# Kernel tuning notes

Measured on AMD Instinct MI355X. Metric: run time of the kernel, lower is better.

The kernel has to match this reference:

```python
import jax, jax.numpy as jnp
import numpy as np
import math

V, D, H, L, T_MAX = 512, 256, 4, 8, 256
HD = D // H
EPS = 1e-5


def _ln(x, g, b):
    mu = jnp.mean(x, axis=-1, keepdims=True)
    var = jnp.mean(jnp.square(x - mu), axis=-1, keepdims=True)
    return (x - mu) * jax.lax.rsqrt(var + EPS) * g + b


def _pos_encoding(T, D):
    pos = jnp.arange(T, dtype=jnp.float32)[:, None]
    div = jnp.exp(jnp.arange(0, D, 2, dtype=jnp.float32) * (-math.log(10000.0) / D))
    pe = jnp.zeros((T, D), dtype=jnp.float32)
    pe = pe.at[:, 0::2].set(jnp.sin(pos * div))
    pe = pe.at[:, 1::2].set(jnp.cos(pos * div))
    return pe


def setup_inputs() -> dict:
    key = jax.random.key(0)
    ks = jax.random.split(key, 16)
    s = 0.02
    B, T = 128, 256
    return {
        "idx": jax.random.randint(ks[0], (B, T), 0, V),
        "tok_emb": jax.random.normal(ks[1], (V, D)) * s,
        "Wq": jax.random.normal(ks[2], (L, D, D)) * s,
        "Wk": jax.random.normal(ks[3], (L, D, D)) * s,
        "Wv": jax.random.normal(ks[4], (L, D, D)) * s,
        "Wo": jax.random.normal(ks[5], (L, D, D)) * s,
        "bo": jnp.zeros((L, D)),
        "W1": jax.random.normal(ks[6], (L, D, D)) * s,
        "b1": jnp.zeros((L, D)),
        "W2": jax.random.normal(ks[7], (L, D, D)) * s,
        "b2": jnp.zeros((L, D)),
        "g1": jnp.ones((L, D)), "be1": jnp.zeros((L, D)),
        "g2": jnp.ones((L, D)), "be2": jnp.zeros((L, D)),
        "gf": jnp.ones((D,)), "bf": jnp.zeros((D,)),
        "Wh": jax.random.normal(ks[8], (D, V)) * s,
        "bh": jnp.zeros((V,)),
    }


def reference(idx, tok_emb, Wq, Wk, Wv, Wo, bo, W1, b1, W2, b2,
              g1, be1, g2, be2, gf, bf, Wh, bh):
    B, T = idx.shape
    x = tok_emb[idx] + _pos_encoding(T, D)[None]  # [B,T,D]
    causal = jnp.tril(jnp.ones((T, T), dtype=bool))
    scale = D ** (-0.5)  # NOTE: original scales by n_embd, not head_size
    for l in range(L):
        h = _ln(x, g1[l], be1[l])
        q = (h @ Wq[l]).reshape(B, T, H, HD)
        k = (h @ Wk[l]).reshape(B, T, H, HD)
        v = (h @ Wv[l]).reshape(B, T, H, HD)
        wei = jnp.einsum('bqhd,bkhd->bhqk', q, k) * scale
        wei = jnp.where(causal, wei, -jnp.inf)
        wei = jax.nn.softmax(wei, axis=-1)
        att = jnp.einsum('bhqk,bkhd->bqhd', wei, v).reshape(B, T, D)
        x = x + att @ Wo[l] + bo[l]
        h = _ln(x, g2[l], be2[l])
        x = x + jax.nn.relu(h @ W1[l] + b1[l]) @ W2[l] + b2[l]
    x = _ln(x, gf, bf)
    logits = x @ Wh + bh  # [B,T,V]
    return logits
```

## Files before the change

kernel.cpp:

```cpp
#include <hip/hip_runtime.h>
#include <hip/hip_bf16.h>

typedef unsigned short u16;
typedef __attribute__((ext_vector_type(8))) short short8;
typedef __attribute__((ext_vector_type(4))) float f32x4;

#define DEV static __device__ __forceinline__

DEV u16 f2bf(float x){
  union { __hip_bfloat16 b; u16 u; } c;
  c.b = __float2bfloat16(x);
  return c.u;
}

DEV void gload16(const void* g, void* lds){
  __builtin_amdgcn_global_load_lds((const __attribute__((address_space(1))) void*)g,
                                   (__attribute__((address_space(3))) void*)lds, 16, 0, 0);
}

__global__ __launch_bounds__(512)
void wconv_kernel(const float* __restrict__ Wq, const float* __restrict__ Wk,
                  const float* __restrict__ Wv, const float* __restrict__ Wo,
                  const float* __restrict__ W1, const float* __restrict__ W2,
                  const float* __restrict__ Wh,
                  u16* __restrict__ WqkvT, u16* __restrict__ WoT,
                  u16* __restrict__ W1T, u16* __restrict__ W2T, u16* __restrict__ WhT)
{
  __shared__ float tile[64][65];
  const int j = blockIdx.y;
  int N = 256;
  const float* src; u16* dst;
  if (j < 48){
    const int li = j / 6, t = j % 6;
    switch(t){
      case 0:  src = Wq + li*65536; dst = WqkvT + li*196608;          break;
      case 1:  src = Wk + li*65536; dst = WqkvT + li*196608 + 65536;  break;
      case 2:  src = Wv + li*65536; dst = WqkvT + li*196608 + 131072; break;
      case 3:  src = Wo + li*65536; dst = WoT  + li*65536;            break;
      case 4:  src = W1 + li*65536; dst = W1T  + li*65536;            break;
      default: src = W2 + li*65536; dst = W2T  + li*65536;            break;
    }
  } else { N = 512; src = Wh; dst = WhT; }
  const int tilesPerRow = N >> 6;
  if ((int)blockIdx.x >= tilesPerRow * 4) return;
  const int tx = blockIdx.x % tilesPerRow, ty = blockIdx.x / tilesPerRow;
  const int tid = threadIdx.x;
  #pragma unroll
  for (int i=0;i<2;++i){
    const int e = tid + i*512;
    const int r = e >> 4, cq = (e & 15)*4;
    float4 v = *(const float4*)(src + (size_t)(ty*64 + r)*N + tx*64 + cq);
    tile[r][cq+0]=v.x; tile[r][cq+1]=v.y; tile[r][cq+2]=v.z; tile[r][cq+3]=v.w;
  }
  __syncthreads();
  #pragma unroll
  for (int i=0;i<2;++i){
    const int e = tid + i*512;
    const int orow = e >> 4, tq = (e & 15)*4;
    ushort4 o;
    o.x = f2bf(tile[tq+0][orow]); o.y = f2bf(tile[tq+1][orow]);
    o.z = f2bf(tile[tq+2][orow]); o.w = f2bf(tile[tq+3][orow]);
    *(ushort4*)(dst + (size_t)(tx*64 + orow)*256 + ty*64 + tq) = o;
  }
}

__global__ __launch_bounds__(256)
void embed_ln_kernel(const int* __restrict__ idx, const float* __restrict__ emb,
                     const float* __restrict__ g, const float* __restrict__ be,
                     float* __restrict__ x, u16* __restrict__ hb)
{
  const int tid = threadIdx.x;
  const int w = tid >> 6, l = tid & 63;
  const int row = blockIdx.x*4 + w;
  const int t = row & 255;
  const int v = idx[row];
  const int c4 = l*4;
  float4 e = *(const float4*)(emb + (size_t)v*256 + c4);
  float r[4];
  const float ef[4] = {e.x, e.y, e.z, e.w};
  #pragma unroll
  for (int i=0;i<4;++i){
    const int c = c4 + i;
    const float div = expf((float)(c & ~1) * (-9.210340371976184f/256.f));
    const float ang = (float)t * div;
    r[i] = ((c & 1) ? cosf(ang) : sinf(ang)) + ef[i];
  }
  *(float4*)(x + (size_t)row*256 + c4) = (float4){r[0],r[1],r[2],r[3]};
  float s = r[0]+r[1]+r[2]+r[3];
  float q = r[0]*r[0]+r[1]*r[1]+r[2]*r[2]+r[3]*r[3];
  #pragma unroll
  for (int m=32; m; m>>=1){ s += __shfl_xor(s,m); q += __shfl_xor(q,m); }
  const float mu = s * (1.f/256.f);
  const float var = q * (1.f/256.f) - mu*mu;
  const float rstd = rsqrtf(var + 1e-5f);
  const float4 gv = *(const float4*)(g + c4);
  const float4 bv = *(const float4*)(be + c4);
  ushort4 o;
  o.x = f2bf((r[0]-mu)*rstd*gv.x + bv.x);
  o.y = f2bf((r[1]-mu)*rstd*gv.y + bv.y);
  o.z = f2bf((r[2]-mu)*rstd*gv.z + bv.z);
  o.w = f2bf((r[3]-mu)*rstd*gv.w + bv.w);
  *(ushort4*)(hb + (size_t)row*256 + c4) = o;
}

template<bool OBF, bool RELU_, bool BIAS_>
__global__ __launch_bounds__(256)
void gemm_kernel(const u16* __restrict__ A, const u16* __restrict__ W,
                 const float* __restrict__ bias, void* __restrict__ Cv, int ldC)
{
  __shared__ __align__(16) u16 Al[2][4096];
  __shared__ __align__(16) u16 Bl[2][4096];
  const int tid = threadIdx.x;
  const int w = tid >> 6, l = tid & 63;
  const int lr = l & 15, lg = l >> 4;
  const int m0 = blockIdx.x * 128, n0 = blockIdx.y * 128;
  const int wm = w >> 1, wn = w & 1;
  const int rowc = l >> 2;
  const int pswz = (l & 3) ^ ((l >> 3) & 3);

  f32x4 acc[4][4];
  #pragma unroll
  for (int i=0;i<4;++i)
    #pragma unroll
    for (int jn=0;jn<4;++jn) acc[i][jn] = (f32x4){0.f,0.f,0.f,0.f};

  #pragma unroll
  for (int cc=0; cc<2; ++cc){
    const int c = w + cc*4;
    gload16(A + (size_t)(m0 + 16*c + rowc)*256 + pswz*8, &Al[0][c*512]);
    gload16(W + (size_t)(n0 + 16*c + rowc)*256 + pswz*8, &Bl[0][c*512]);
  }
  __syncthreads();

  for (int kt=0; kt<8; ++kt){
    if (kt < 7){
      const int kofs = (kt+1) * 32, nb = (kt+1) & 1;
      #pragma unroll
      for (int cc=0; cc<2; ++cc){
        const int c = w + cc*4;
        gload16(A + (size_t)(m0 + 16*c + rowc)*256 + kofs + pswz*8, &Al[nb][c*512]);
        gload16(W + (size_t)(n0 + 16*c + rowc)*256 + kofs + pswz*8, &Bl[nb][c*512]);
      }
    }
    const int buf = kt & 1;
    short8 af[4], bf[4];
    #pragma unroll
    for (int mt=0; mt<4; ++mt){
      const int row = wm*64 + mt*16 + lr;
      const int kb = (lg*16) ^ ((((row>>1)&3))<<4);
      af[mt] = *(const short8*)((const char*)Al[buf] + row*64 + kb);
    }
    #pragma unroll
    for (int nt=0; nt<4; ++nt){
      const int row = wn*64 + nt*16 + lr;
      const int kb = (lg*16) ^ ((((row>>1)&3))<<4);
      bf[nt] = *(const short8*)((const char*)Bl[buf] + row*64 + kb);
    }
    #pragma unroll
    for (int mt=0; mt<4; ++mt)
      #pragma unroll
      for (int nt=0; nt<4; ++nt)
        acc[mt][nt] = __builtin_amdgcn_mfma_f32_16x16x32_bf16(af[mt], bf[nt], acc[mt][nt], 0,0,0);
    __syncthreads();
  }

  #pragma unroll
  for (int nt=0; nt<4; ++nt){
    const int col = n0 + wn*64 + nt*16 + lr;
    const float bv = BIAS_ ? bias[col] : 0.f;
    #pragma unroll
    for (int mt=0; mt<4; ++mt){
      f32x4 v = acc[mt][nt];
      #pragma unroll
      for (int r=0;r<4;++r){
        const int row = m0 + wm*64 + mt*16 + lg*4 + r;
        float val = v[r] + bv;
        if (RELU_) val = fmaxf(val, 0.f);
        if (OBF) ((u16*)Cv)[(size_t)row*ldC + col] = f2bf(val);
        else     ((float*)Cv)[(size_t)row*ldC + col] = val;
      }
    }
  }
}

__global__ __launch_bounds__(256, 2)
void gemm_res_ln_kernel(const u16* __restrict__ A, const u16* __restrict__ W,
                        const float* __restrict__ bias,
                        const float* __restrict__ g, const float* __restrict__ be,
                        float* __restrict__ x, u16* __restrict__ hb)
{
  __shared__ __align__(16) u16 Al[2][2048];
  __shared__ __align__(16) u16 Bl[2][8192];
  __shared__ float sS[64][2], sQ[64][2];
  const int tid = threadIdx.x;
  const int w = tid >> 6, l = tid & 63;
  const int lr = l & 15, lg = l >> 4;
  const int m0 = blockIdx.x * 64;
  const int wm = w >> 1, wn = w & 1;
  const int rowc = l >> 2;
  const int pswz = (l & 3) ^ ((l >> 3) & 3);

  f32x4 acc[2][2][4];
  #pragma unroll
  for (int p=0;p<2;++p)
    #pragma unroll
    for (int i=0;i<2;++i)
      #pragma unroll
      for (int jn=0;jn<4;++jn) acc[p][i][jn] = (f32x4){0.f,0.f,0.f,0.f};

  gload16(A + (size_t)(m0 + 16*w + rowc)*256 + pswz*8, &Al[0][w*512]);
  #pragma unroll
  for (int cc=0; cc<4; ++cc){
    const int c = w + cc*4;
    gload16(W + (size_t)(16*c + rowc)*256 + pswz*8, &Bl[0][c*512]);
  }
  __syncthreads();

  for (int kt=0; kt<8; ++kt){
    if (kt < 7){
      const int kofs = (kt+1)*32, nb = (kt+1)&1;
      gload16(A + (size_t)(m0 + 16*w + rowc)*256 + kofs + pswz*8, &Al[nb][w*512]);
      #pragma unroll
      for (int cc=0; cc<4; ++cc){
        const int c = w + cc*4;
        gload16(W + (size_t)(16*c + rowc)*256 + kofs + pswz*8, &Bl[nb][c*512]);
      }
    }
    const int buf = kt & 1;
    short8 af[2], bf[2][4];
    #pragma unroll
    for (int mt=0; mt<2; ++mt){
      const int row = wm*32 + mt*16 + lr;
      const int kb = (lg*16) ^ ((((row>>1)&3))<<4);
      af[mt] = *(const short8*)((const char*)Al[buf] + row*64 + kb);
    }
    #pragma unroll
    for (int p=0; p<2; ++p)
      #pragma unroll
      for (int nt=0; nt<4; ++nt){
        const int brow = p*128 + wn*64 + nt*16 + lr;
        const int kb = (lg*16) ^ ((((brow>>1)&3))<<4);
        bf[p][nt] = *(const short8*)((const char*)Bl[buf] + brow*64 + kb);
      }
    #pragma unroll
    for (int p=0; p<2; ++p)
      #pragma unroll
      for (int mt=0; mt<2; ++mt)
        #pragma unroll
        for (int nt=0; nt<4; ++nt)
          acc[p][mt][nt] = __builtin_amdgcn_mfma_f32_16x16x32_bf16(af[mt], bf[p][nt], acc[p][mt][nt], 0,0,0);
    __syncthreads();
  }

  float bcol[2][4], gcol[2][4], becol[2][4];
  #pragma unroll
  for (int p=0;p<2;++p)
    #pragma unroll
    for (int nt=0;nt<4;++nt){
      const int col = p*128 + wn*64 + nt*16 + lr;
      bcol[p][nt] = bias[col]; gcol[p][nt] = g[col]; becol[p][nt] = be[col];
    }
  float s8[2][4], q8[2][4];
  #pragma unroll
  for (int mt=0;mt<2;++mt)
    #pragma unroll
    for (int rr=0;rr<4;++rr){ s8[mt][rr]=0.f; q8[mt][rr]=0.f; }

  #pragma unroll
  for (int p=0;p<2;++p)
    #pragma unroll
    for (int mt=0;mt<2;++mt)
      #pragma unroll
      for (int nt=0;nt<4;++nt)
        #pragma unroll
        for (int rr=0;rr<4;++rr){
          const int row = m0 + wm*32 + mt*16 + lg*4 + rr;
          const int col = p*128 + wn*64 + nt*16 + lr;
          float val = acc[p][mt][nt][rr] + bcol[p][nt] + x[(size_t)row*256 + col];
          x[(size_t)row*256 + col] = val;
          acc[p][mt][nt][rr] = val;
          s8[mt][rr] += val; q8[mt][rr] += val*val;
        }
  #pragma unroll
  for (int mt=0;mt<2;++mt)
    #pragma unroll
    for (int rr=0;rr<4;++rr){
      #pragma unroll
      for (int m=1; m<16; m<<=1){
        s8[mt][rr] += __shfl_xor(s8[mt][rr], m);
        q8[mt][rr] += __shfl_xor(q8[mt][rr], m);
      }
      if (lr == 0){
        const int lrow = wm*32 + mt*16 + lg*4 + rr;
        sS[lrow][wn] = s8[mt][rr]; sQ[lrow][wn] = q8[mt][rr];
      }
    }
  __syncthreads();

  #pragma unroll
  for (int mt=0;mt<2;++mt)
    #pragma unroll
    for (int rr=0;rr<4;++rr){
      const int lrow = wm*32 + mt*16 + lg*4 + rr;
      const float mu = (sS[lrow][0] + sS[lrow][1]) * (1.f/256.f);
      const float var = (sQ[lrow][0] + sQ[lrow][1]) * (1.f/256.f) - mu*mu;
      const float rstd = rsqrtf(var + 1e-5f);
      #pragma unroll
      for (int p=0;p<2;++p)
        #pragma unroll
        for (int nt=0;nt<4;++nt){
          const int col = p*128 + wn*64 + nt*16 + lr;
          const float out = (acc[p][mt][nt][rr] - mu)*rstd*gcol[p][nt] + becol[p][nt];
          hb[(size_t)(m0+lrow)*256 + col] = f2bf(out);
        }
    }
}

__global__ __launch_bounds__(512, 4)
void attn_kernel(const u16* __restrict__ qkv, u16* __restrict__ att)
{
  __shared__ __align__(16) u16 sK[16384];
  __shared__ __align__(16) u16 sV[16384];
  __shared__ __align__(16) u16 sP[8192];
  const int bh = blockIdx.x;
  const int b = bh >> 2, h = bh & 3;
  const int tid = threadIdx.x;
  const int w = tid >> 6, l = tid & 63, lr = l & 15, lg = l >> 4;
  const u16* base = qkv + (size_t)(b*256)*768;

  #pragma unroll
  for (int it=0; it<4; ++it){
    const int c = tid + it*512;
    const int t = c >> 3, p = c & 7;
    uint4 val = *(const uint4*)(base + (size_t)t*768 + 256 + h*64 + p*8);
    *(uint4*)((char*)sK + t*128 + ((p*16) ^ ((t&7)<<4))) = val;
  }
  #pragma unroll
  for (int h2=0; h2<2; ++h2){
    #pragma unroll
    for (int i=0;i<2;++i){
      const int e = tid + i*512;
      const int t2 = e >> 3, p = e & 7;
      uint4 val = *(const uint4*)(base + (size_t)(h2*128 + t2)*768 + 512 + h*64 + p*8);
      *(uint4*)((char*)sP + t2*128 + ((p*16) ^ ((t2&7)<<4))) = val;
    }
    __syncthreads();
    {
      const int tq2 = tid >> 4, hq = tid & 15;
      ushort4 vv[4];
      #pragma unroll
      for (int i=0;i<4;++i){
        const int t2 = tq2*4 + i;
        vv[i] = *(const ushort4*)((char*)sP + t2*128 +
                   (((hq>>1)*16) ^ ((t2&7)<<4)) + (hq&1)*8);
      }
      const int tqg = h2*32 + tq2;
      #pragma unroll
      for (int i2=0;i2<4;++i2){
        const int hd = hq*4 + i2;
        ushort4 o;
        o.x = ((const u16*)&vv[0])[i2]; o.y = ((const u16*)&vv[1])[i2];
        o.z = ((const u16*)&vv[2])[i2]; o.w = ((const u16*)&vv[3])[i2];
        *(ushort4*)((char*)sV + hd*512 + ((tqg*8) ^ ((hd&31)<<4))) = o;
      }
    }
    __syncthreads();
  }

  char* sPw = (char*)sP + w*2048;
  const int swzq = (lr & 7) << 4;
  u16* ab = att + (size_t)(b*256)*256 + h*64;
  const float c1 = 0.09016844005556021f;

  #pragma unroll
  for (int ph=0; ph<2; ++ph){
    const int rt = ph ? (15 - w) : w;
    const u16* qp = base + (size_t)(rt*16 + lr)*768 + h*64;
    const short8 qf0 = *(const short8*)(qp + lg*8);
    const short8 qf1 = *(const short8*)(qp + 32 + lg*8);

    f32x4 acc[16];
    #pragma unroll
    for (int nt=0; nt<16; ++nt) acc[nt] = (f32x4){0.f,0.f,0.f,0.f};
    #pragma unroll
    for (int nt=0; nt<16; ++nt){
      if (nt <= rt){
        const int row = nt*16 + lr;
        const int swz = (row & 7) << 4;
        short8 k0 = *(const short8*)((const char*)sK + row*128 + ((lg*16) ^ swz));
        short8 k1 = *(const short8*)((const char*)sK + row*128 + ((64 + lg*16) ^ swz));
        acc[nt] = __builtin_amdgcn_mfma_f32_16x16x32_bf16(k0, qf0, acc[nt], 0,0,0);
        acc[nt] = __builtin_amdgcn_mfma_f32_16x16x32_bf16(k1, qf1, acc[nt], 0,0,0);
      }
    }
    #pragma unroll
    for (int nt=0; nt<16; ++nt){
      if (nt == rt){
        #pragma unroll
        for (int r=0;r<4;++r)
          acc[nt][r] = (lg*4 + r > lr) ? -3.0e38f : acc[nt][r];
      }
    }

    float m_ = -3.0e38f;
    #pragma unroll
    for (int nt=0; nt<16; ++nt){
      if (nt <= rt){
        float t01 = fmaxf(acc[nt][0], acc[nt][1]);
        float t23 = fmaxf(acc[nt][2], acc[nt][3]);
        m_ = fmaxf(m_, fmaxf(t01, t23));
      }
    }
    m_ = fmaxf(m_, __shfl_xor(m_, 16));
    m_ = fmaxf(m_, __shfl_xor(m_, 32));
    const float mm = m_ * c1;
    float s_ = 0.f;
    #pragma unroll
    for (int nt=0; nt<16; ++nt){
      if (nt <= rt){
        #pragma unroll
        for (int r=0;r<4;++r){
          const float p = exp2f(fmaf(acc[nt][r], c1, -mm));
          acc[nt][r] = p;
          s_ += p;
        }
      }
    }
    s_ += __shfl_xor(s_, 16);
    s_ += __shfl_xor(s_, 32);
    const float inv = 1.f / s_;

    f32x4 oacc[4];
    #pragma unroll
    for (int nt=0; nt<4; ++nt) oacc[nt] = (f32x4){0.f,0.f,0.f,0.f};
    #pragma unroll
    for (int c=0; c<4; ++c){
      if (c <= (rt >> 2)){
        #pragma unroll
        for (int e=0; e<4; ++e){
          const int nt = 4*c + e;
          ushort4 pk;
          #pragma unroll
          for (int r=0;r<4;++r){
            const float val = (nt <= rt) ? acc[nt][r] * inv : 0.f;
            ((u16*)&pk)[r] = f2bf(val);
          }
          *(ushort4*)(sPw + lr*128 + ((e*32 + lg*8) ^ swzq)) = pk;
        }
        #pragma unroll
        for (int kc=0; kc<2; ++kc){
          const int tc = 2*c + kc;
          if (tc <= (rt >> 1)){
            const short8 ap = *(const short8*)(sPw + lr*128 + ((kc*64 + lg*16) ^ swzq));
            #pragma unroll
            for (int nt=0; nt<4; ++nt){
              const int vrow = nt*16 + lr;
              const short8 bv = *(const short8*)((const char*)sV + vrow*512 +
                                   ((tc*64 + lg*16) ^ ((vrow&31)<<4)));
              oacc[nt] = __builtin_amdgcn_mfma_f32_16x16x32_bf16(ap, bv, oacc[nt], 0,0,0);
            }
          }
        }
      }
    }

    #pragma unroll
    for (int nt=0; nt<4; ++nt)
      #pragma unroll
      for (int r=0;r<4;++r){
        const int row = rt*16 + lg*4 + r;
        ab[(size_t)row*256 + nt*16 + lr] = f2bf(oacc[nt][r]);
      }
  }
}

extern "C" void kernel_launch(void* const* d_in, const int* in_sizes, int n_in,
                              void* d_out, int out_size, void* d_ws, size_t ws_size,
                              hipStream_t stream)
{
  (void)in_sizes; (void)n_in; (void)out_size; (void)ws_size;
  const int*   idx = (const int*)  d_in[0];
  const float* tok = (const float*)d_in[1];
  const float* Wq  = (const float*)d_in[2];
  const float* Wk  = (const float*)d_in[3];
  const float* Wv  = (const float*)d_in[4];
  const float* Wo  = (const float*)d_in[5];
  const float* bo  = (const float*)d_in[6];
  const float* W1  = (const float*)d_in[7];
  const float* b1  = (const float*)d_in[8];
  const float* W2  = (const float*)d_in[9];
  const float* b2  = (const float*)d_in[10];
  const float* g1  = (const float*)d_in[11];
  const float* be1 = (const float*)d_in[12];
  const float* g2  = (const float*)d_in[13];
  const float* be2 = (const float*)d_in[14];
  const float* gf  = (const float*)d_in[15];
  const float* bfi = (const float*)d_in[16];
  const float* Wh  = (const float*)d_in[17];
  const float* bh  = (const float*)d_in[18];

  char* ws = (char*)d_ws;
  float* x    = (float*)ws;  ws += (size_t)32768*256*4;
  u16*   hb   = (u16*)ws;    ws += (size_t)32768*256*2;
  u16*   mid  = (u16*)ws;    ws += (size_t)32768*256*2;
  u16*   qkv  = (u16*)ws;    ws += (size_t)32768*768*2;
  u16*   att  = (u16*)ws;    ws += (size_t)32768*256*2;
  u16*   WqkvT= (u16*)ws;    ws += (size_t)8*768*256*2;
  u16*   WoT  = (u16*)ws;    ws += (size_t)8*256*256*2;
  u16*   W1T  = (u16*)ws;    ws += (size_t)8*256*256*2;
  u16*   W2T  = (u16*)ws;    ws += (size_t)8*256*256*2;
  u16*   WhT  = (u16*)ws;    ws += (size_t)512*256*2;

  wconv_kernel<<<dim3(32,49),512,0,stream>>>(Wq,Wk,Wv,Wo,W1,W2,Wh,WqkvT,WoT,W1T,W2T,WhT);
  embed_ln_kernel<<<8192,256,0,stream>>>(idx, tok, g1, be1, x, hb);
  for (int l=0; l<8; ++l){
    gemm_kernel<true,false,false><<<dim3(256,6),256,0,stream>>>(
        hb, WqkvT + (size_t)l*196608, nullptr, qkv, 768);
    attn_kernel<<<512,512,0,stream>>>(qkv, att);
    gemm_res_ln_kernel<<<512,256,0,stream>>>(
        att, WoT + (size_t)l*65536, bo + l*256, g2 + l*256, be2 + l*256, x, hb);
    gemm_kernel<true,true,true><<<dim3(256,2),256,0,stream>>>(
        hb, W1T + (size_t)l*65536, b1 + l*256, mid, 256);
    const float* gn = (l < 7) ? (g1 + (l+1)*256) : gf;
    const float* bn = (l < 7) ? (be1 + (l+1)*256) : bfi;
    gemm_res_ln_kernel<<<512,256,0,stream>>>(
        mid, W2T + (size_t)l*65536, b2 + l*256, gn, bn, x, hb);
  }
  gemm_kernel<false,false,true><<<dim3(256,4),256,0,stream>>>(
      hb, WhT, bh, (float*)d_out, 512);
}
```

Before: 869.0 us.

## Fuse QKV projection into attention kernel, drop qkv buffer round trip

```diff
diff --git a/kernel.cpp b/kernel.cpp
--- a/kernel.cpp
+++ b/kernel.cpp
@@ -317,7 +317,8 @@
 }
 
 __global__ __launch_bounds__(512, 4)
-void attn_kernel(const u16* __restrict__ qkv, u16* __restrict__ att)
+void fused_qkv_attn_kernel(const u16* __restrict__ hb, const u16* __restrict__ Wqkv,
+                           u16* __restrict__ att)
 {
   __shared__ __align__(16) u16 sK[16384];
   __shared__ __align__(16) u16 sV[16384];
@@ -326,46 +327,72 @@
   const int b = bh >> 2, h = bh & 3;
   const int tid = threadIdx.x;
   const int w = tid >> 6, l = tid & 63, lr = l & 15, lg = l >> 4;
-  const u16* base = qkv + (size_t)(b*256)*768;
-
-  #pragma unroll
-  for (int it=0; it<4; ++it){
-    const int c = tid + it*512;
-    const int t = c >> 3, p = c & 7;
-    uint4 val = *(const uint4*)(base + (size_t)t*768 + 256 + h*64 + p*8);
-    *(uint4*)((char*)sK + t*128 + ((p*16) ^ ((t&7)<<4))) = val;
-  }
-  #pragma unroll
-  for (int h2=0; h2<2; ++h2){
-    #pragma unroll
-    for (int i=0;i<2;++i){
-      const int e = tid + i*512;
-      const int t2 = e >> 3, p = e & 7;
-      uint4 val = *(const uint4*)(base + (size_t)(h2*128 + t2)*768 + 512 + h*64 + p*8);
-      *(uint4*)((char*)sP + t2*128 + ((p*16) ^ ((t2&7)<<4))) = val;
-    }
-    __syncthreads();
-    {
-      const int tq2 = tid >> 4, hq = tid & 15;
-      ushort4 vv[4];
-      #pragma unroll
-      for (int i=0;i<4;++i){
-        const int t2 = tq2*4 + i;
-        vv[i] = *(const ushort4*)((char*)sP + t2*128 +
-                   (((hq>>1)*16) ^ ((t2&7)<<4)) + (hq&1)*8);
-      }
-      const int tqg = h2*32 + tq2;
-      #pragma unroll
-      for (int i2=0;i2<4;++i2){
-        const int hd = hq*4 + i2;
-        ushort4 o;
-        o.x = ((const u16*)&vv[0])[i2]; o.y = ((const u16*)&vv[1])[i2];
-        o.z = ((const u16*)&vv[2])[i2]; o.w = ((const u16*)&vv[3])[i2];
-        *(ushort4*)((char*)sV + hd*512 + ((tqg*8) ^ ((hd&31)<<4))) = o;
-      }
-    }
-    __syncthreads();
-  }
+  const u16* hbb = hb + (size_t)(b*256)*256;
+  const u16* Wq_ = Wqkv + (size_t)(h*64)*256;
+  const u16* Wk_ = Wqkv + 65536 + (size_t)(h*64)*256;
+  const u16* Wv_ = Wqkv + 131072 + (size_t)(h*64)*256;
+
+  {
+    f32x4 pacc[4][4];
+    #pragma unroll
+    for (int i=0;i<4;++i)
+      #pragma unroll
+      for (int jn=0;jn<4;++jn) pacc[i][jn] = (f32x4){0.f,0.f,0.f,0.f};
+    if (w < 4){
+      const int t0 = w*64;
+      for (int kt=0; kt<8; ++kt){
+        short8 af[4], bf[4];
+        #pragma unroll
+        for (int mt=0; mt<4; ++mt)
+          af[mt] = *(const short8*)(Wk_ + (size_t)(mt*16+lr)*256 + kt*32 + lg*8);
+        #pragma unroll
+        for (int nt=0; nt<4; ++nt)
+          bf[nt] = *(const short8*)(hbb + (size_t)(t0+nt*16+lr)*256 + kt*32 + lg*8);
+        #pragma unroll
+        for (int mt=0; mt<4; ++mt)
+          #pragma unroll
+          for (int nt=0; nt<4; ++nt)
+            pacc[mt][nt] = __builtin_amdgcn_mfma_f32_16x16x32_bf16(af[mt], bf[nt], pacc[mt][nt], 0,0,0);
+      }
+      #pragma unroll
+      for (int mt=0; mt<4; ++mt)
+        #pragma unroll
+        for (int nt=0; nt<4; ++nt){
+          const int t = t0 + nt*16 + lr;
+          ushort4 o;
+          o.x = f2bf(pacc[mt][nt][0]); o.y = f2bf(pacc[mt][nt][1]);
+          o.z = f2bf(pacc[mt][nt][2]); o.w = f2bf(pacc[mt][nt][3]);
+          *(ushort4*)((char*)sK + t*128 + ((mt*32 + lg*8) ^ ((t&7)<<4))) = o;
+        }
+    } else {
+      const int t0 = (w-4)*64;
+      for (int kt=0; kt<8; ++kt){
+        short8 af[4], bf[4];
+        #pragma unroll
+        for (int mt=0; mt<4; ++mt)
+          af[mt] = *(const short8*)(hbb + (size_t)(t0+mt*16+lr)*256 + kt*32 + lg*8);
+        #pragma unroll
+        for (int nt=0; nt<4; ++nt)
+          bf[nt] = *(const short8*)(Wv_ + (size_t)(nt*16+lr)*256 + kt*32 + lg*8);
+        #pragma unroll
+        for (int mt=0; mt<4; ++mt)
+          #pragma unroll
+          for (int nt=0; nt<4; ++nt)
+            pacc[mt][nt] = __builtin_amdgcn_mfma_f32_16x16x32_bf16(af[mt], bf[nt], pacc[mt][nt], 0,0,0);
+      }
+      #pragma unroll
+      for (int mt=0; mt<4; ++mt)
+        #pragma unroll
+        for (int nt=0; nt<4; ++nt){
+          const int d = nt*16 + lr;
+          ushort4 o;
+          o.x = f2bf(pacc[mt][nt][0]); o.y = f2bf(pacc[mt][nt][1]);
+          o.z = f2bf(pacc[mt][nt][2]); o.w = f2bf(pacc[mt][nt][3]);
+          *(ushort4*)((char*)sV + d*512 + (((t0 + mt*16 + lg*4)*2) ^ ((d&31)<<4))) = o;
+        }
+    }
+  }
+  __syncthreads();
 
   char* sPw = (char*)sP + w*2048;
   const int swzq = (lr & 7) << 4;
@@ -375,9 +402,29 @@
   #pragma unroll
   for (int ph=0; ph<2; ++ph){
     const int rt = ph ? (15 - w) : w;
-    const u16* qp = base + (size_t)(rt*16 + lr)*768 + h*64;
-    const short8 qf0 = *(const short8*)(qp + lg*8);
-    const short8 qf1 = *(const short8*)(qp + 32 + lg*8);
+
+    {
+      f32x4 qacc[4];
+      #pragma unroll
+      for (int mt=0; mt<4; ++mt) qacc[mt] = (f32x4){0.f,0.f,0.f,0.f};
+      for (int kt=0; kt<8; ++kt){
+        const short8 bq = *(const short8*)(hbb + (size_t)(rt*16+lr)*256 + kt*32 + lg*8);
+        #pragma unroll
+        for (int mt=0; mt<4; ++mt){
+          const short8 aq = *(const short8*)(Wq_ + (size_t)(mt*16+lr)*256 + kt*32 + lg*8);
+          qacc[mt] = __builtin_amdgcn_mfma_f32_16x16x32_bf16(aq, bq, qacc[mt], 0,0,0);
+        }
+      }
+      #pragma unroll
+      for (int mt=0; mt<4; ++mt){
+        ushort4 o;
+        o.x = f2bf(qacc[mt][0]); o.y = f2bf(qacc[mt][1]);
+        o.z = f2bf(qacc[mt][2]); o.w = f2bf(qacc[mt][3]);
+        *(ushort4*)(sPw + lr*128 + ((mt*32 + lg*8) ^ swzq)) = o;
+      }
+    }
+    const short8 qf0 = *(const short8*)(sPw + lr*128 + ((lg*16) ^ swzq));
+    const short8 qf1 = *(const short8*)(sPw + lr*128 + ((64 + lg*16) ^ swzq));
 
     f32x4 acc[16];
     #pragma unroll
@@ -503,7 +550,6 @@
   float* x    = (float*)ws;  ws += (size_t)32768*256*4;
   u16*   hb   = (u16*)ws;    ws += (size_t)32768*256*2;
   u16*   mid  = (u16*)ws;    ws += (size_t)32768*256*2;
-  u16*   qkv  = (u16*)ws;    ws += (size_t)32768*768*2;
   u16*   att  = (u16*)ws;    ws += (size_t)32768*256*2;
   u16*   WqkvT= (u16*)ws;    ws += (size_t)8*768*256*2;
   u16*   WoT  = (u16*)ws;    ws += (size_t)8*256*256*2;
@@ -514,9 +560,7 @@
   wconv_kernel<<<dim3(32,49),512,0,stream>>>(Wq,Wk,Wv,Wo,W1,W2,Wh,WqkvT,WoT,W1T,W2T,WhT);
   embed_ln_kernel<<<8192,256,0,stream>>>(idx, tok, g1, be1, x, hb);
   for (int l=0; l<8; ++l){
-    gemm_kernel<true,false,false><<<dim3(256,6),256,0,stream>>>(
-        hb, WqkvT + (size_t)l*196608, nullptr, qkv, 768);
-    attn_kernel<<<512,512,0,stream>>>(qkv, att);
+    fused_qkv_attn_kernel<<<512,512,0,stream>>>(hb, WqkvT + (size_t)l*196608, att);
     gemm_res_ln_kernel<<<512,256,0,stream>>>(
         att, WoT + (size_t)l*65536, bo + l*256, g2 + l*256, be2 + l*256, x, hb);
     gemm_kernel<true,true,true><<<dim3(256,2),256,0,stream>>>(
```

New measurement: 1.076 ms. +23.8%, slower.

## Store residual stream in bf16 and simplify V transpose staging in attention

Applied to the files above, without the earlier changes.

```diff
diff --git a/kernel.cpp b/kernel.cpp
--- a/kernel.cpp
+++ b/kernel.cpp
@@ -11,6 +11,11 @@
   union { __hip_bfloat16 b; u16 u; } c;
   c.b = __float2bfloat16(x);
   return c.u;
+}
+DEV float bf2f(u16 u){
+  union { float f; unsigned i; } c;
+  c.i = ((unsigned)u) << 16;
+  return c.f;
 }
 
 DEV void gload16(const void* g, void* lds){
@@ -67,7 +72,7 @@
 __global__ __launch_bounds__(256)
 void embed_ln_kernel(const int* __restrict__ idx, const float* __restrict__ emb,
                      const float* __restrict__ g, const float* __restrict__ be,
-                     float* __restrict__ x, u16* __restrict__ hb)
+                     u16* __restrict__ x, u16* __restrict__ hb)
 {
   const int tid = threadIdx.x;
   const int w = tid >> 6, l = tid & 63;
@@ -85,7 +90,9 @@
     const float ang = (float)t * div;
     r[i] = ((c & 1) ? cosf(ang) : sinf(ang)) + ef[i];
   }
-  *(float4*)(x + (size_t)row*256 + c4) = (float4){r[0],r[1],r[2],r[3]};
+  ushort4 xo;
+  xo.x = f2bf(r[0]); xo.y = f2bf(r[1]); xo.z = f2bf(r[2]); xo.w = f2bf(r[3]);
+  *(ushort4*)(x + (size_t)row*256 + c4) = xo;
   float s = r[0]+r[1]+r[2]+r[3];
   float q = r[0]*r[0]+r[1]*r[1]+r[2]*r[2]+r[3]*r[3];
   #pragma unroll
@@ -187,7 +194,7 @@
 void gemm_res_ln_kernel(const u16* __restrict__ A, const u16* __restrict__ W,
                         const float* __restrict__ bias,
                         const float* __restrict__ g, const float* __restrict__ be,
-                        float* __restrict__ x, u16* __restrict__ hb)
+                        u16* __restrict__ x, u16* __restrict__ hb)
 {
   __shared__ __align__(16) u16 Al[2][2048];
   __shared__ __align__(16) u16 Bl[2][8192];
@@ -276,8 +283,9 @@
         for (int rr=0;rr<4;++rr){
           const int row = m0 + wm*32 + mt*16 + lg*4 + rr;
           const int col = p*128 + wn*64 + nt*16 + lr;
-          float val = acc[p][mt][nt][rr] + bcol[p][nt] + x[(size_t)row*256 + col];
-          x[(size_t)row*256 + col] = val;
+          float val = acc[p][mt][nt][rr] + bcol[p][nt] + bf2f(x[(size_t)row*256 + col]);
+          x[(size_t)row*256 + col] = f2bf(val);
+          val = bf2f(f2bf(val));
           acc[p][mt][nt][rr] = val;
           s8[mt][rr] += val; q8[mt][rr] += val*val;
         }
@@ -336,36 +344,17 @@
     *(uint4*)((char*)sK + t*128 + ((p*16) ^ ((t&7)<<4))) = val;
   }
   #pragma unroll
-  for (int h2=0; h2<2; ++h2){
-    #pragma unroll
-    for (int i=0;i<2;++i){
-      const int e = tid + i*512;
-      const int t2 = e >> 3, p = e & 7;
-      uint4 val = *(const uint4*)(base + (size_t)(h2*128 + t2)*768 + 512 + h*64 + p*8);
-      *(uint4*)((char*)sP + t2*128 + ((p*16) ^ ((t2&7)<<4))) = val;
-    }
-    __syncthreads();
-    {
-      const int tq2 = tid >> 4, hq = tid & 15;
-      ushort4 vv[4];
-      #pragma unroll
-      for (int i=0;i<4;++i){
-        const int t2 = tq2*4 + i;
-        vv[i] = *(const ushort4*)((char*)sP + t2*128 +
-                   (((hq>>1)*16) ^ ((t2&7)<<4)) + (hq&1)*8);
-      }
-      const int tqg = h2*32 + tq2;
-      #pragma unroll
-      for (int i2=0;i2<4;++i2){
-        const int hd = hq*4 + i2;
-        ushort4 o;
-        o.x = ((const u16*)&vv[0])[i2]; o.y = ((const u16*)&vv[1])[i2];
-        o.z = ((const u16*)&vv[2])[i2]; o.w = ((const u16*)&vv[3])[i2];
-        *(ushort4*)((char*)sV + hd*512 + ((tqg*8) ^ ((hd&31)<<4))) = o;
-      }
-    }
-    __syncthreads();
-  }
+  for (int it=0; it<8; ++it){
+    const int c = tid + it*512;
+    const int t = c >> 4, hdq = c & 15;
+    ushort4 v = *(const ushort4*)(base + (size_t)t*768 + 512 + h*64 + hdq*4);
+    #pragma unroll
+    for (int j=0;j<4;++j){
+      const int hd = hdq*4 + j;
+      *(u16*)((char*)sV + hd*512 + ((t*2) ^ ((hd&31)<<4))) = ((const u16*)&v)[j];
+    }
+  }
+  __syncthreads();
 
   char* sPw = (char*)sP + w*2048;
   const int swzq = (lr & 7) << 4;
@@ -500,7 +489,7 @@
   const float* bh  = (const float*)d_in[18];
 
   char* ws = (char*)d_ws;
-  float* x    = (float*)ws;  ws += (size_t)32768*256*4;
+  u16*   x    = (u16*)ws;    ws += (size_t)32768*256*2;
   u16*   hb   = (u16*)ws;    ws += (size_t)32768*256*2;
   u16*   mid  = (u16*)ws;    ws += (size_t)32768*256*2;
   u16*   qkv  = (u16*)ws;    ws += (size_t)32768*768*2;
```

After: 795.0 us. 1.09x faster.
